# Kernel optimization log

Measured on AMD Instinct MI355X. Metric: run time of the kernel, lower is better.

## Reference

```python
import jax, jax.numpy as jnp
import numpy as np

HEADS = 16
DIM_HEAD = 64
QUERY_DIM = 1024


def setup_inputs() -> dict:
    key = jax.random.key(0)
    ks = jax.random.split(key, 5)
    B, S, D = 4, 2048, QUERY_DIM
    inner = HEADS * DIM_HEAD
    s = 0.02
    return {
        "x": jax.random.normal(ks[0], (B, S, D), dtype=jnp.float32),
        "Wq": jax.random.normal(ks[1], (D, inner), dtype=jnp.float32) * s,
        "Wk": jax.random.normal(ks[2], (D, inner), dtype=jnp.float32) * s,
        "Wv": jax.random.normal(ks[3], (D, inner), dtype=jnp.float32) * s,
        "Wo": jax.random.normal(ks[4], (inner, D), dtype=jnp.float32) * s,
    }


def reference(x, Wq, Wk, Wv, Wo):
    B, S, D = x.shape
    h, d = HEADS, DIM_HEAD
    scale = d ** (-0.5)
    # projections -> [B, h, S, d]
    q = (x @ Wq).reshape(B, S, h, d).transpose(0, 2, 1, 3)
    k = (x @ Wk).reshape(B, S, h, d).transpose(0, 2, 1, 3)
    v = (x @ Wv).reshape(B, S, h, d).transpose(0, 2, 1, 3)
    # scores [B, h, S, S]
    attn = jnp.einsum("bhqd,bhkd->bhqk", q, k) * scale
    attn = jax.nn.softmax(attn, axis=-1)
    out = jnp.einsum("bhqk,bhkd->bhqd", attn, v)
    out = out.transpose(0, 2, 1, 3).reshape(B, S, h * d)
    return out @ Wo
```

## Files before the change

kernel.cpp:

```cpp
#include <hip/hip_runtime.h>
#include <cstddef>

#define BATCH  4
#define SLEN   2048
#define NHEADS 16
#define DHEAD  64
#define DMODEL 1024

typedef __attribute__((ext_vector_type(8)))  short short8;
typedef __attribute__((ext_vector_type(4)))  float f32x4;
typedef __attribute__((ext_vector_type(16))) float f32x16;

__device__ inline unsigned short f2bf(float f) {
    union { float f; unsigned int u; } v; v.f = f;
    unsigned int r = v.u + 0x7fffu + ((v.u >> 16) & 1u);
    return (unsigned short)(r >> 16);
}

__device__ inline float fast_exp2(float x) {
#if __has_builtin(__builtin_amdgcn_exp2f)
    return __builtin_amdgcn_exp2f(x);
#else
    return __expf(x * 0.69314718f);
#endif
}

__device__ inline void gload_lds16(const unsigned short* g, unsigned short* l) {
    __builtin_amdgcn_global_load_lds(
        (const __attribute__((address_space(1))) void*)g,
        (__attribute__((address_space(3))) void*)l, 16, 0, 0);
}

__global__ __launch_bounds__(256)
void prep(const float* __restrict__ x, unsigned short* __restrict__ xb,
          const float* __restrict__ W0, const float* __restrict__ W1,
          const float* __restrict__ W2, const float* __restrict__ W3,
          unsigned short* __restrict__ T0, unsigned short* __restrict__ T1,
          unsigned short* __restrict__ T2, unsigned short* __restrict__ T3)
{
    __shared__ unsigned short T[64 * 72];
    const int bid = blockIdx.x;
    const int tid = threadIdx.x;

    if (bid < 4096) {
        const int i = bid * 256 + tid;
        const float4 a = ((const float4*)x)[2 * i];
        const float4 b = ((const float4*)x)[2 * i + 1];
        short8 o;
        o[0] = (short)f2bf(a.x); o[1] = (short)f2bf(a.y);
        o[2] = (short)f2bf(a.z); o[3] = (short)f2bf(a.w);
        o[4] = (short)f2bf(b.x); o[5] = (short)f2bf(b.y);
        o[6] = (short)f2bf(b.z); o[7] = (short)f2bf(b.w);
        ((short8*)xb)[i] = o;
        return;
    }

    const int idx = bid - 4096;
    const int z = idx >> 8;
    const float* W = (z == 0) ? W0 : (z == 1) ? W1 : (z == 2) ? W2 : W3;
    unsigned short* Wt = (z == 0) ? T0 : (z == 1) ? T1 : (z == 2) ? T2 : T3;
    const int n0 = (idx & 15) * 64, k0 = ((idx >> 4) & 15) * 64;

    #pragma unroll
    for (int it = 0; it < 2; it++) {
        const int t2 = it * 256 + tid;
        const int row = t2 >> 3, col8 = (t2 & 7) * 8;
        const float4 a = *(const float4*)(W + (size_t)(k0 + row) * DMODEL + n0 + col8);
        const float4 b = *(const float4*)(W + (size_t)(k0 + row) * DMODEL + n0 + col8 + 4);
        short8 o;
        o[0] = (short)f2bf(a.x); o[1] = (short)f2bf(a.y);
        o[2] = (short)f2bf(a.z); o[3] = (short)f2bf(a.w);
        o[4] = (short)f2bf(b.x); o[5] = (short)f2bf(b.y);
        o[6] = (short)f2bf(b.z); o[7] = (short)f2bf(b.w);
        *(short8*)&T[row * 72 + col8] = o;
    }
    __syncthreads();
    #pragma unroll
    for (int it = 0; it < 2; it++) {
        const int t2 = it * 256 + tid;
        const int nn = t2 >> 3, k8 = (t2 & 7) * 8;
        short8 v;
        #pragma unroll
        for (int j = 0; j < 8; j++) v[j] = (short)T[(k8 + j) * 72 + nn];
        *(short8*)(Wt + (size_t)(n0 + nn) * DMODEL + k0 + k8) = v;
    }
}

template<int KIND>
__global__ __launch_bounds__(256)
void gemm_bf16(const unsigned short* __restrict__ A,
               const unsigned short* __restrict__ B0,
               const unsigned short* __restrict__ B1,
               const unsigned short* __restrict__ B2,
               void* __restrict__ C0v, void* __restrict__ C1v, void* __restrict__ C2v)
{
    constexpr int N = DMODEL, K = DMODEL;
    __shared__ unsigned short As[128 * 64];
    __shared__ unsigned short Bs[128 * 64];

    const int z = blockIdx.z;
    const unsigned short* Bw = (z == 0) ? B0 : (z == 1) ? B1 : B2;
    void* Cv = (z == 0) ? C0v : (z == 1) ? C1v : C2v;

    const int tid  = threadIdx.x;
    const int lane = tid & 63;
    const int wave = tid >> 6;
    const int c  = lane & 15, qd = lane >> 4;
    const int wr = wave >> 1, wc = wave & 1;
    const int m0 = blockIdx.y * 128, n0 = blockIdx.x * 128;

    const unsigned short* ag[4];
    const unsigned short* bg[4];
    unsigned short* al[4];
    unsigned short* bl[4];
    #pragma unroll
    for (int j = 0; j < 4; j++) {
        const int cid = j * 256 + tid;
        const int row = cid >> 3;
        const int k8  = (cid & 7) ^ (row & 7);
        ag[j] = A  + (size_t)(m0 + row) * K + k8 * 8;
        bg[j] = Bw + (size_t)(n0 + row) * K + k8 * 8;
        al[j] = &As[cid * 8];
        bl[j] = &Bs[cid * 8];
    }

    f32x4 acc[4][4];
    #pragma unroll
    for (int mb = 0; mb < 4; mb++)
        #pragma unroll
        for (int nb = 0; nb < 4; nb++)
            #pragma unroll
            for (int r = 0; r < 4; r++) acc[mb][nb][r] = 0.f;

    for (int k0 = 0; k0 < K; k0 += 64) {
        __syncthreads();
        #pragma unroll
        for (int j = 0; j < 4; j++) {
            gload_lds16(ag[j], al[j]);
            gload_lds16(bg[j], bl[j]);
            ag[j] += 64; bg[j] += 64;
        }
        __syncthreads();

        #pragma unroll
        for (int ks = 0; ks < 2; ks++) {
            const int sw = (ks * 4 + qd) ^ (c & 7);
            short8 af[4], bf[4];
            #pragma unroll
            for (int mb = 0; mb < 4; mb++)
                af[mb] = *(const short8*)&As[((wr * 64 + mb * 16 + c) * 8 + sw) * 8];
            #pragma unroll
            for (int nb = 0; nb < 4; nb++)
                bf[nb] = *(const short8*)&Bs[((wc * 64 + nb * 16 + c) * 8 + sw) * 8];
            #pragma unroll
            for (int mb = 0; mb < 4; mb++)
                #pragma unroll
                for (int nb = 0; nb < 4; nb++)
                    acc[mb][nb] = __builtin_amdgcn_mfma_f32_16x16x32_bf16(
                        af[mb], bf[nb], acc[mb][nb], 0, 0, 0);
        }
    }

    const int mbase = m0 + wr * 64 + qd * 4;
    const int nbase = n0 + wc * 64 + c;
    if (KIND == 1) {
        float* C = (float*)Cv;
        #pragma unroll
        for (int mb = 0; mb < 4; mb++)
            #pragma unroll
            for (int nb = 0; nb < 4; nb++)
                #pragma unroll
                for (int r = 0; r < 4; r++)
                    C[(size_t)(mbase + mb * 16 + r) * N + nbase + nb * 16] = acc[mb][nb][r];
    } else if (z != 2) {
        unsigned short* C = (unsigned short*)Cv;
        const float osc = (z == 0) ? 0.18033688f : 1.0f;
        #pragma unroll
        for (int mb = 0; mb < 4; mb++)
            #pragma unroll
            for (int nb = 0; nb < 4; nb++)
                #pragma unroll
                for (int r = 0; r < 4; r++)
                    C[(size_t)(mbase + mb * 16 + r) * N + nbase + nb * 16] =
                        f2bf(acc[mb][nb][r] * osc);
    } else {
        unsigned short* C = (unsigned short*)Cv;
        const int b = mbase >> 11;
        #pragma unroll
        for (int mb = 0; mb < 4; mb++) {
            const int s = (mbase + mb * 16) & 2047;
            #pragma unroll
            for (int nb = 0; nb < 4; nb++) {
                const int n = nbase + nb * 16;
                const int h = n >> 6, dd = n & 63;
                ushort4 val = make_ushort4(f2bf(acc[mb][nb][0]), f2bf(acc[mb][nb][1]),
                                           f2bf(acc[mb][nb][2]), f2bf(acc[mb][nb][3]));
                *(ushort4*)(C + ((size_t)((b * 16 + h) * 64 + dd)) * SLEN + s) = val;
            }
        }
    }
}

__global__ __launch_bounds__(256, 4)
void attn_mfma9(const unsigned short* __restrict__ qb,
                const unsigned short* __restrict__ kb,
                const unsigned short* __restrict__ vtb,
                unsigned short* __restrict__ O)
{
    __shared__ unsigned short lds[16384];
    unsigned short* Ks = lds;
    unsigned short* Vs = lds + 8192;

    const int tid = threadIdx.x;
    const int w   = tid >> 6, ln = tid & 63;
    const int c5  = ln & 31;
    const int l5i = ln >> 5;

    const int L  = blockIdx.x + (int)gridDim.x * blockIdx.y;
    const int wg = (L & 7) * 128 + (L >> 3);
    const int qt = wg & 15, bh = wg >> 4;
    const int b = bh >> 4, h = bh & 15;
    const size_t bh_base = ((size_t)b * SLEN * NHEADS + h) * 64;
    constexpr int RS = NHEADS * 64;

    const int srow = ln >> 3;
    const int sk8  = (ln & 7) ^ srow;
    const int prow = (srow & 3) | ((w & 1) << 2) | (((srow >> 2) & 1) << 3) | ((w >> 1) << 4);
    const unsigned short* kg0 = kb + bh_base + (size_t)prow * RS + sk8 * 8;
    const unsigned short* kg1 = kg0 + (size_t)32 * RS;
    const unsigned short* vg0 = vtb + ((size_t)bh * 64 + w * 8 + srow) * SLEN + sk8 * 8;
    const unsigned short* vg1 = vg0 + (size_t)32 * SLEN;
    unsigned short* kl0 = &Ks[(w * 64 + ln) * 8];
    unsigned short* kl1 = kl0 + 2048;
    unsigned short* vl0 = &Vs[(w * 64 + ln) * 8];
    unsigned short* vl1 = vl0 + 2048;

    const int qtile = qt * 128 + w * 32;

    short8 qf[4];
    #pragma unroll
    for (int kst = 0; kst < 4; kst++)
        qf[kst] = *(const short8*)(qb + bh_base +
            (size_t)(qtile + c5) * RS + kst * 16 + l5i * 8);

    f32x16 acc[2];
    #pragma unroll
    for (int db = 0; db < 2; db++)
        #pragma unroll
        for (int r = 0; r < 16; r++) acc[db][r] = 0.f;
    float lsum = 0.f;
    const int cl7 = c5 & 7;

    gload_lds16(kg0, kl0); gload_lds16(kg1, kl1);
    gload_lds16(vg0, vl0); gload_lds16(vg1, vl1);
    kg0 += (size_t)64 * RS; kg1 += (size_t)64 * RS; vg0 += 64; vg1 += 64;
    __syncthreads();

    for (int kt = 0; kt < SLEN / 64; kt++) {
        const int buf = kt & 1;
        if (kt < SLEN / 64 - 1) {
            const int nb = (buf ^ 1) * 4096;
            gload_lds16(kg0, kl0 + nb); gload_lds16(kg1, kl1 + nb);
            gload_lds16(vg0, vl0 + nb); gload_lds16(vg1, vl1 + nb);
            kg0 += (size_t)64 * RS; kg1 += (size_t)64 * RS; vg0 += 64; vg1 += 64;
        }
        const unsigned short* Kb = Ks + buf * 4096;
        const unsigned short* Vb = Vs + buf * 4096;

        #pragma unroll
        for (int kb32 = 0; kb32 < 2; kb32++) {
            f32x16 sacc;
            #pragma unroll
            for (int r = 0; r < 16; r++) sacc[r] = 0.f;
            __builtin_amdgcn_s_setprio(1);
            #pragma unroll
            for (int kst = 0; kst < 4; kst++) {
                const int slot = (kst * 2 + l5i) ^ cl7;
                short8 kf = *(const short8*)&Kb[((kb32 * 32 + c5) * 8 + slot) * 8];
                sacc = __builtin_amdgcn_mfma_f32_32x32x16_bf16(
                    kf, qf[kst], sacc, 0, 0, 0);
            }
            __builtin_amdgcn_s_setprio(0);

            unsigned pk[8];
            {
                float p[16];
                float s0 = 0.f, s1 = 0.f;
                #pragma unroll
                for (int r = 0; r < 16; r += 2) {
                    p[r]     = fast_exp2(sacc[r]);
                    p[r + 1] = fast_exp2(sacc[r + 1]);
                    s0 += p[r]; s1 += p[r + 1];
                }
                lsum += s0 + s1;
                #pragma unroll
                for (int i = 0; i < 8; i++)
                    pk[i] = __builtin_amdgcn_perm(
                        __float_as_uint(p[2 * i + 1]), __float_as_uint(p[2 * i]),
                        0x07060302u);
            }

            #pragma unroll
            for (int kk = 0; kk < 2; kk++) {
                const int k2 = kb32 * 2 + kk;
                union { unsigned u[4]; short8 s; } t;
                t.u[0] = pk[4 * kk + 0];
                t.u[1] = pk[4 * kk + 1];
                t.u[2] = pk[4 * kk + 2];
                t.u[3] = pk[4 * kk + 3];
                const short8 pf = t.s;
                __builtin_amdgcn_s_setprio(1);
                #pragma unroll
                for (int db = 0; db < 2; db++) {
                    const int slot = (k2 * 2 + l5i) ^ cl7;
                    short8 vf = *(const short8*)&Vb[((db * 32 + c5) * 8 + slot) * 8];
                    acc[db] = __builtin_amdgcn_mfma_f32_32x32x16_bf16(
                        vf, pf, acc[db], 0, 0, 0);
                }
                __builtin_amdgcn_s_setprio(0);
            }
        }
        __syncthreads();
    }

    float l = lsum;
    l += __shfl_xor(l, 32);
    const float inv = 1.001953125f / l;
    unsigned short* E = lds + w * 2304;
    #pragma unroll
    for (int db = 0; db < 2; db++)
        #pragma unroll
        for (int u = 0; u < 4; u++) {
            const int d0 = db * 32 + 8 * u + 4 * l5i;
            const int q  = c5;
            ushort4 val = make_ushort4(
                f2bf(acc[db][4 * u + 0] * inv),
                f2bf(acc[db][4 * u + 1] * inv),
                f2bf(acc[db][4 * u + 2] * inv),
                f2bf(acc[db][4 * u + 3] * inv));
            *(ushort4*)&E[q * 72 + d0] = val;
        }
    __builtin_amdgcn_wave_barrier();
    #pragma unroll
    for (int it = 0; it < 4; it++) {
        const int t2 = it * 64 + ln;
        const int row = t2 >> 3, col8 = (t2 & 7) * 8;
        short8 o = *(const short8*)&E[row * 72 + col8];
        *(short8*)(O + bh_base + (size_t)(qtile + row) * RS + col8) = o;
    }
}

extern "C" void kernel_launch(void* const* d_in, const int* in_sizes, int n_in,
                              void* d_out, int out_size, void* d_ws, size_t ws_size,
                              hipStream_t stream)
{
    const float* x  = (const float*)d_in[0];
    const float* Wq = (const float*)d_in[1];
    const float* Wk = (const float*)d_in[2];
    const float* Wv = (const float*)d_in[3];
    const float* Wo = (const float*)d_in[4];
    float* out = (float*)d_out;

    const size_t per = (size_t)BATCH * SLEN * NHEADS * DHEAD;
    const size_t wsz = (size_t)DMODEL * DMODEL;
    unsigned short* qb  = (unsigned short*)d_ws;
    unsigned short* kb  = qb  + per;
    unsigned short* vtb = kb  + per;
    unsigned short* xb  = vtb + per;
    unsigned short* wtq = xb  + per;
    unsigned short* wtk = wtq + wsz;
    unsigned short* wtv = wtk + wsz;
    unsigned short* wto = wtv + wsz;

    dim3 blk(256);
    prep<<<dim3(4096 + 1024), blk, 0, stream>>>(x, xb, Wq, Wk, Wv, Wo,
                                                wtq, wtk, wtv, wto);

    gemm_bf16<0><<<dim3(8, 64, 3), blk, 0, stream>>>(xb, wtq, wtk, wtv, qb, kb, vtb);

    attn_mfma9<<<dim3(SLEN / 128, BATCH * NHEADS), blk, 0, stream>>>(qb, kb, vtb, qb);

    gemm_bf16<1><<<dim3(8, 64, 1), blk, 0, stream>>>(qb, wto, wto, wto, out, out, out);
}
```

Measured before the change: 264.0 us.

## Stage V-transpose epilogue through LDS and single-buffer attention K/V tiles

```diff
diff --git a/kernel.cpp b/kernel.cpp
--- a/kernel.cpp
+++ b/kernel.cpp
@@ -95,8 +95,9 @@
                void* __restrict__ C0v, void* __restrict__ C1v, void* __restrict__ C2v)
 {
     constexpr int N = DMODEL, K = DMODEL;
-    __shared__ unsigned short As[128 * 64];
-    __shared__ unsigned short Bs[128 * 64];
+    __shared__ unsigned short lds[17408];
+    unsigned short* As = lds;
+    unsigned short* Bs = lds + 8192;
 
     const int z = blockIdx.z;
     const unsigned short* Bw = (z == 0) ? B0 : (z == 1) ? B1 : B2;
@@ -184,32 +185,45 @@
                     C[(size_t)(mbase + mb * 16 + r) * N + nbase + nb * 16] =
                         f2bf(acc[mb][nb][r] * osc);
     } else {
-        unsigned short* C = (unsigned short*)Cv;
-        const int b = mbase >> 11;
+        __syncthreads();
+        unsigned short* T = lds;
         #pragma unroll
         for (int mb = 0; mb < 4; mb++) {
-            const int s = (mbase + mb * 16) & 2047;
+            const int sl = wr * 64 + qd * 4 + mb * 16;
             #pragma unroll
             for (int nb = 0; nb < 4; nb++) {
-                const int n = nbase + nb * 16;
-                const int h = n >> 6, dd = n & 63;
+                const int dl = wc * 64 + nb * 16 + c;
                 ushort4 val = make_ushort4(f2bf(acc[mb][nb][0]), f2bf(acc[mb][nb][1]),
                                            f2bf(acc[mb][nb][2]), f2bf(acc[mb][nb][3]));
-                *(ushort4*)(C + ((size_t)((b * 16 + h) * 64 + dd)) * SLEN + s) = val;
+                *(ushort4*)&T[dl * 136 + sl] = val;
             }
         }
+        __syncthreads();
+        unsigned short* C = (unsigned short*)Cv;
+        const int b  = m0 >> 11;
+        const int s0 = m0 & 2047;
+        #pragma unroll
+        for (int it = 0; it < 8; it++) {
+            const int chunk = it * 256 + tid;
+            const int row  = chunk >> 4;
+            const int col8 = (chunk & 15) * 8;
+            const int n = n0 + row;
+            const int h2 = n >> 6, dd = n & 63;
+            short8 v = *(const short8*)&T[row * 136 + col8];
+            *(short8*)(C + ((size_t)((b * 16 + h2) * 64 + dd)) * SLEN + s0 + col8) = v;
+        }
     }
 }
 
 __global__ __launch_bounds__(256, 4)
-void attn_mfma9(const unsigned short* __restrict__ qb,
+void attn_mfma6(const unsigned short* __restrict__ qb,
                 const unsigned short* __restrict__ kb,
                 const unsigned short* __restrict__ vtb,
                 unsigned short* __restrict__ O)
 {
-    __shared__ unsigned short lds[16384];
+    __shared__ unsigned short lds[18432];
     unsigned short* Ks = lds;
-    unsigned short* Vs = lds + 8192;
+    unsigned short* Vs = lds + 4096;
 
     const int tid = threadIdx.x;
     const int w   = tid >> 6, ln = tid & 63;
@@ -251,21 +265,12 @@
     float lsum = 0.f;
     const int cl7 = c5 & 7;
 
-    gload_lds16(kg0, kl0); gload_lds16(kg1, kl1);
-    gload_lds16(vg0, vl0); gload_lds16(vg1, vl1);
-    kg0 += (size_t)64 * RS; kg1 += (size_t)64 * RS; vg0 += 64; vg1 += 64;
-    __syncthreads();
-
     for (int kt = 0; kt < SLEN / 64; kt++) {
-        const int buf = kt & 1;
-        if (kt < SLEN / 64 - 1) {
-            const int nb = (buf ^ 1) * 4096;
-            gload_lds16(kg0, kl0 + nb); gload_lds16(kg1, kl1 + nb);
-            gload_lds16(vg0, vl0 + nb); gload_lds16(vg1, vl1 + nb);
-            kg0 += (size_t)64 * RS; kg1 += (size_t)64 * RS; vg0 += 64; vg1 += 64;
-        }
-        const unsigned short* Kb = Ks + buf * 4096;
-        const unsigned short* Vb = Vs + buf * 4096;
+        __syncthreads();
+        gload_lds16(kg0, kl0); gload_lds16(kg1, kl1);
+        gload_lds16(vg0, vl0); gload_lds16(vg1, vl1);
+        kg0 += (size_t)64 * RS; kg1 += (size_t)64 * RS; vg0 += 64; vg1 += 64;
+        __syncthreads();
 
         #pragma unroll
         for (int kb32 = 0; kb32 < 2; kb32++) {
@@ -276,7 +281,7 @@
             #pragma unroll
             for (int kst = 0; kst < 4; kst++) {
                 const int slot = (kst * 2 + l5i) ^ cl7;
-                short8 kf = *(const short8*)&Kb[((kb32 * 32 + c5) * 8 + slot) * 8];
+                short8 kf = *(const short8*)&Ks[((kb32 * 32 + c5) * 8 + slot) * 8];
                 sacc = __builtin_amdgcn_mfma_f32_32x32x16_bf16(
                     kf, qf[kst], sacc, 0, 0, 0);
             }
@@ -313,16 +318,16 @@
                 #pragma unroll
                 for (int db = 0; db < 2; db++) {
                     const int slot = (k2 * 2 + l5i) ^ cl7;
-                    short8 vf = *(const short8*)&Vb[((db * 32 + c5) * 8 + slot) * 8];
+                    short8 vf = *(const short8*)&Vs[((db * 32 + c5) * 8 + slot) * 8];
                     acc[db] = __builtin_amdgcn_mfma_f32_32x32x16_bf16(
                         vf, pf, acc[db], 0, 0, 0);
                 }
                 __builtin_amdgcn_s_setprio(0);
             }
         }
-        __syncthreads();
-    }
-
+    }
+
+    __syncthreads();
     float l = lsum;
     l += __shfl_xor(l, 32);
     const float inv = 1.001953125f / l;
@@ -378,7 +383,7 @@
 
     gemm_bf16<0><<<dim3(8, 64, 3), blk, 0, stream>>>(xb, wtq, wtk, wtv, qb, kb, vtb);
 
-    attn_mfma9<<<dim3(SLEN / 128, BATCH * NHEADS), blk, 0, stream>>>(qb, kb, vtb, qb);
+    attn_mfma6<<<dim3(SLEN / 128, BATCH * NHEADS), blk, 0, stream>>>(qb, kb, vtb, qb);
 
     gemm_bf16<1><<<dim3(8, 64, 1), blk, 0, stream>>>(qb, wto, wto, wto, out, out, out);
 }
```

Result: no change. 262.6 us (-0.5%).
